# Kernel tuning notes

Hardware: AMD Instinct MI355X
Metric: run time of the kernel (lower is better)

## Reference

```python
import jax, jax.numpy as jnp
import numpy as np

N = 100_000          # nodes
E = 3_200_000        # edges (avg degree 32)
USER_SIZE = 80_000
CAT_SIZE = 5_000
USER_DIM = 8
CAT_DIM = 4
IN_CH = 8
OUT_CH = 16
HID = 16


def setup_inputs() -> dict:
    key = jax.random.key(0)
    ks = jax.random.split(key, 24)
    # features: [N,3] int; col0 = id (user id if type==0 else category id), col1 = known flag in {0,1}, col2 = type in {0,1}
    typ = jax.random.randint(ks[0], (N,), 0, 2)
    uid = jax.random.randint(ks[1], (N,), 0, USER_SIZE)
    cid = jax.random.randint(ks[2], (N,), 0, CAT_SIZE)
    col0 = jnp.where(typ == 0, uid, cid)
    col1 = jax.random.randint(ks[3], (N,), 0, 2)
    features = jnp.stack([col0, col1, typ], axis=1).astype(jnp.int64)
    edges = jax.random.randint(ks[4], (2, E), 0, N).astype(jnp.int64)

    def p(k, shape):
        return jax.random.normal(k, shape, dtype=jnp.float32) * 0.1

    return {
        "edges": edges,
        "features": features,
        "emb_user": p(ks[5], (USER_SIZE, USER_DIM)),
        "emb_known": p(ks[6], (2, USER_DIM)),
        "w_user": p(ks[7], (USER_DIM, IN_CH)),
        "b_user": p(ks[8], (IN_CH,)),
        "emb_cat": p(ks[9], (CAT_SIZE, CAT_DIM)),
        "w_cat": p(ks[10], (CAT_DIM, IN_CH)),
        "b_cat": p(ks[11], (IN_CH,)),
        "w0": p(ks[12], (IN_CH, HID)),
        "b0": p(ks[13], (HID,)),
        "w2": p(ks[14], (HID, OUT_CH)),
        "b2": p(ks[15], (OUT_CH,)),
        "w_node": p(ks[16], (OUT_CH, 2)),
        "b_node": p(ks[17], (2,)),
        "w_mem": p(ks[18], (OUT_CH, 1)),
        "b_mem": p(ks[19], (1,)),
    }


def _gcn_conv(x, w, b, src, dst, edge_norm, self_norm, n):
    h = x @ w                                      # [N, out]
    msgs = h[src] * edge_norm[:, None]             # [E, out] gather + scale
    agg = jax.ops.segment_sum(msgs, dst, num_segments=n)  # scatter-add
    agg = agg + h * self_norm[:, None]             # self-loop term
    return agg + b


def reference(edges, features, emb_user, emb_known, w_user, b_user, emb_cat,
              w_cat, b_cat, w0, b0, w2, b2, w_node, b_node, w_mem, b_mem):
    n = features.shape[0]
    typ = features[:, -1]
    is_user = (typ == 0)

    # --- input encoding (masked gather/scatter expressed as dense select) ---
    uidx = jnp.clip(features[:, 0], 0, emb_user.shape[0] - 1)
    kidx = jnp.clip(features[:, 1], 0, 1)
    cidx = jnp.clip(features[:, 0], 0, emb_cat.shape[0] - 1)
    user_f = jax.nn.relu(emb_user[uidx] + emb_known[kidx]) @ w_user + b_user
    cat_f = jax.nn.relu(emb_cat[cidx]) @ w_cat + b_cat
    x = jnp.where(is_user[:, None], user_f, cat_f)  # [N, IN_CH]

    # --- GCN normalization (shared across layers) ---
    src, dst = edges[0], edges[1]
    deg = jax.ops.segment_sum(jnp.ones((src.shape[0],), x.dtype), dst,
                              num_segments=n) + 1.0  # +1 for self-loop
    dinv = jax.lax.rsqrt(deg)
    edge_norm = dinv[src] * dinv[dst]
    self_norm = dinv * dinv

    # NOTE: original forward loop skips layers[1] entirely (enumerate over layers[:-2],
    # then applies layers[-1]); dropout branch (i>1) never triggers. Faithful here.
    h = jax.nn.relu(_gcn_conv(x, w0, b0, src, dst, edge_norm, self_norm, n))
    h = jax.nn.relu(_gcn_conv(h, w2, b2, src, dst, edge_norm, self_norm, n))

    member_pred = h @ w_mem + b_mem   # [N, 1]
    node_pred = h @ w_node + b_node   # [N, 2]
    return (member_pred, node_pred)
```

## Files before the change

### kernel.cpp

```cpp
#include <hip/hip_runtime.h>
#include <hip/hip_fp16.h>

#define BLK 256
#define PBLK 1024
#define NPB 256
#define NBSHIFT 7
#define BNODES 128
#define BMASK 127
#define NBMAX 800
#define CAP 8192
#define FXS 1048576.0f
#define FXI (1.0f / 1048576.0f)

typedef int v4i __attribute__((ext_vector_type(4)));

static inline int cdiv(int a, int b) { return (a + b - 1) / b; }

__global__ void __launch_bounds__(PBLK)
k_hist(const int* __restrict__ dst, int* __restrict__ histG, int e, int nb) {
    __shared__ int h[NBMAX];
    int tid = threadIdx.x;
    for (int t = tid; t < nb; t += PBLK) h[t] = 0;
    __syncthreads();
    int per = ((e + (int)gridDim.x - 1) / (int)gridDim.x + 3) & ~3;
    int beg = blockIdx.x * per;
    int end = min(e, beg + per);
    if (beg < end) {
        int m4 = beg + ((end - beg) & ~3);
        for (int i = beg + tid * 4; i < m4; i += PBLK * 4) {
            v4i d4 = __builtin_nontemporal_load((const v4i*)(dst + i));
            atomicAdd(&h[d4[0] >> NBSHIFT], 1);
            atomicAdd(&h[d4[1] >> NBSHIFT], 1);
            atomicAdd(&h[d4[2] >> NBSHIFT], 1);
            atomicAdd(&h[d4[3] >> NBSHIFT], 1);
        }
        int it = m4 + tid;
        if (it < end) atomicAdd(&h[dst[it] >> NBSHIFT], 1);
    }
    __syncthreads();
    for (int t = tid; t < nb; t += PBLK) histG[(size_t)blockIdx.x * nb + t] = h[t];
}

__global__ void __launch_bounds__(NPB)
k_base(const int* __restrict__ histG, int* __restrict__ baseG, int* __restrict__ tot, int nb) {
    __shared__ int s[NPB];
    int b = blockIdx.x;
    int t = threadIdx.x;
    int hc = histG[(size_t)t * nb + b];
    int r = (hc + 15) & ~15;
    s[t] = r;
    __syncthreads();
    for (int off = 1; off < NPB; off <<= 1) {
        int v = (t >= off) ? s[t - off] : 0;
        __syncthreads();
        s[t] += v;
        __syncthreads();
    }
    int excl = s[t] - r;
    baseG[(size_t)t * nb + b] = b * CAP + excl;
    if (t == NPB - 1) tot[b] = min(s[t], CAP);
}

__global__ void __launch_bounds__(PBLK)
k_scatter(const int* __restrict__ src, const int* __restrict__ dst,
          const int* __restrict__ baseG, int* __restrict__ slab, int e, int nb) {
    __shared__ int cur[NBMAX];
    int tid = threadIdx.x;
    int blk = blockIdx.x;
    for (int t = tid; t < nb; t += PBLK) cur[t] = baseG[(size_t)blk * nb + t];
    __syncthreads();
    int per = ((e + (int)gridDim.x - 1) / (int)gridDim.x + 3) & ~3;
    int beg = blk * per;
    int end = min(e, beg + per);
    if (beg < end) {
        int m4 = beg + ((end - beg) & ~3);
        for (int i = beg + tid * 4; i < m4; i += PBLK * 4) {
            v4i s4 = __builtin_nontemporal_load((const v4i*)(src + i));
            v4i d4 = __builtin_nontemporal_load((const v4i*)(dst + i));
#pragma unroll
            for (int k = 0; k < 4; ++k) {
                int d = d4[k];
                int b = d >> NBSHIFT;
                int pos = atomicAdd(&cur[b], 1);
                if (pos < (b + 1) * CAP) slab[pos] = (s4[k] << NBSHIFT) | (d & BMASK);
            }
        }
        int it = m4 + tid;
        if (it < end) {
            int d = dst[it];
            int b = d >> NBSHIFT;
            int pos = atomicAdd(&cur[b], 1);
            if (pos < (b + 1) * CAP) slab[pos] = (src[it] << NBSHIFT) | (d & BMASK);
        }
    }
    __syncthreads();
    for (int bb = tid; bb < nb; bb += PBLK) {
        int c = cur[bb];
        int lim = (bb + 1) * CAP;
        while ((c & 15) && c < lim) slab[c++] = -1;
    }
}

__global__ void __launch_bounds__(BLK)
k_bdeg(const int* __restrict__ tot, const int* __restrict__ slab,
       float* __restrict__ dinv, int n) {
    __shared__ int cnt[BNODES];
    int tid = threadIdx.x;
    if (tid < BNODES) cnt[tid] = 0;
    __syncthreads();
    int b = blockIdx.x;
    int nslots = tot[b] >> 2;
    const v4i* sl4 = reinterpret_cast<const v4i*>(slab + (size_t)b * CAP);
    for (int i = tid; i < nslots; i += BLK) {
        v4i u4 = sl4[i];
#pragma unroll
        for (int k = 0; k < 4; ++k)
            if (u4[k] >= 0) atomicAdd(&cnt[u4[k] & BMASK], 1);
    }
    __syncthreads();
    int nd = b * BNODES + tid;
    if (tid < BNODES && nd < n) dinv[nd] = rsqrtf((float)cnt[tid] + 1.0f);
}

__global__ void k_featmm(const int* __restrict__ feat,
                         const float* __restrict__ emb_user,
                         const float* __restrict__ emb_known,
                         const float* __restrict__ w_user,
                         const float* __restrict__ b_user,
                         const float* __restrict__ emb_cat,
                         const float* __restrict__ w_cat,
                         const float* __restrict__ b_cat,
                         const float* __restrict__ w0,
                         const float* __restrict__ dinv,
                         __half* __restrict__ Hs,
                         int n, int user_max, int cat_max) {
    __shared__ float w0s[8 * 16];
    for (int t = threadIdx.x; t < 8 * 16; t += blockDim.x) w0s[t] = w0[t];
    __syncthreads();
    int i = blockIdx.x * blockDim.x + threadIdx.x;
    if (i >= n) return;
    int col0 = feat[i * 3 + 0];
    int col1 = feat[i * 3 + 1];
    int typ  = feat[i * 3 + 2];
    float x[8];
    if (typ == 0) {
        int u = min(max(col0, 0), user_max);
        int k = min(max(col1, 0), 1);
        const float4* eu = reinterpret_cast<const float4*>(emb_user + (size_t)u * 8);
        const float4* ek = reinterpret_cast<const float4*>(emb_known + (size_t)k * 8);
        float4 a0 = eu[0], a1 = eu[1], k0 = ek[0], k1 = ek[1];
        float in[8];
        in[0] = fmaxf(a0.x + k0.x, 0.f); in[1] = fmaxf(a0.y + k0.y, 0.f);
        in[2] = fmaxf(a0.z + k0.z, 0.f); in[3] = fmaxf(a0.w + k0.w, 0.f);
        in[4] = fmaxf(a1.x + k1.x, 0.f); in[5] = fmaxf(a1.y + k1.y, 0.f);
        in[6] = fmaxf(a1.z + k1.z, 0.f); in[7] = fmaxf(a1.w + k1.w, 0.f);
#pragma unroll
        for (int c = 0; c < 8; ++c) {
            float s = b_user[c];
#pragma unroll
            for (int d = 0; d < 8; ++d) s += in[d] * w_user[d * 8 + c];
            x[c] = s;
        }
    } else {
        int ci = min(max(col0, 0), cat_max);
        float4 c0 = reinterpret_cast<const float4*>(emb_cat + (size_t)ci * 4)[0];
        float in[4];
        in[0] = fmaxf(c0.x, 0.f); in[1] = fmaxf(c0.y, 0.f);
        in[2] = fmaxf(c0.z, 0.f); in[3] = fmaxf(c0.w, 0.f);
#pragma unroll
        for (int c = 0; c < 8; ++c) {
            float s = b_cat[c];
#pragma unroll
            for (int d = 0; d < 4; ++d) s += in[d] * w_cat[d * 8 + c];
            x[c] = s;
        }
    }
    float dv = dinv[i];
    float o[16];
#pragma unroll
    for (int c = 0; c < 16; ++c) {
        float s = 0.f;
#pragma unroll
        for (int d = 0; d < 8; ++d) s += x[d] * w0s[d * 16 + c];
        o[c] = s * dv;
    }
    union { __half2 h[8]; uint4 u[2]; } pk;
#pragma unroll
    for (int k = 0; k < 8; ++k) pk.h[k] = __floats2half2_rn(o[2 * k], o[2 * k + 1]);
    uint4* dp = reinterpret_cast<uint4*>(Hs + (size_t)i * 16);
    dp[0] = pk.u[0];
    dp[1] = pk.u[1];
}

__device__ __forceinline__ void gather_loop(const int* __restrict__ slabb, int mtot,
                                            const uint4* __restrict__ Hs4,
                                            int (*acc)[17], int tid) {
    const v4i* sl4 = reinterpret_cast<const v4i*>(slabb);
    int nslots = mtot >> 2;
    int g = tid >> 1, q = tid & 1;
    for (int base = 0; base < nslots; base += 256) {
        int i0 = base + g;
        int i1 = base + 128 + g;
        v4i e0 = sl4[min(i0, (CAP >> 2) - 1)];
        v4i e1 = sl4[min(i1, (CAP >> 2) - 1)];
        bool b0 = i0 < nslots, b1 = i1 < nslots;
        int us[8];
        us[0] = b0 ? e0[0] : -1; us[1] = b0 ? e0[1] : -1;
        us[2] = b0 ? e0[2] : -1; us[3] = b0 ? e0[3] : -1;
        us[4] = b1 ? e1[0] : -1; us[5] = b1 ? e1[1] : -1;
        us[6] = b1 ? e1[2] : -1; us[7] = b1 ? e1[3] : -1;
        uint4 v[8];
#pragma unroll
        for (int k = 0; k < 8; ++k)
            if (us[k] >= 0) v[k] = Hs4[(size_t)(us[k] >> NBSHIFT) * 2 + q];
#pragma unroll
        for (int k = 0; k < 8; ++k) {
            if (us[k] >= 0) {
                int dl = us[k] & BMASK;
                union { uint4 u4; __half2 h[4]; } c;
                c.u4 = v[k];
#pragma unroll
                for (int j = 0; j < 4; ++j) {
                    float2 f = __half22float2(c.h[j]);
                    atomicAdd(&acc[dl][8 * q + 2 * j + 0], __float2int_rn(f.x * FXS));
                    atomicAdd(&acc[dl][8 * q + 2 * j + 1], __float2int_rn(f.y * FXS));
                }
            }
        }
    }
}

__global__ void __launch_bounds__(BLK, 4)
k_bconv1(const int* __restrict__ tot, const int* __restrict__ slab,
         const __half* __restrict__ Hs, const float* __restrict__ dinv,
         const float* __restrict__ b0, const float* __restrict__ w2,
         __half* __restrict__ Hs2, int n) {
    __shared__ int acc[BNODES][17];
    __shared__ float w2s[16 * 16];
    __shared__ float b0s[16];
    int tid = threadIdx.x;
    for (int t = tid; t < BNODES * 17; t += BLK) ((int*)acc)[t] = 0;
    w2s[tid] = w2[tid];
    if (tid < 16) b0s[tid] = b0[tid];
    __syncthreads();
    int b = blockIdx.x;
    gather_loop(slab + (size_t)b * CAP, tot[b], reinterpret_cast<const uint4*>(Hs), acc, tid);
    __syncthreads();
    int nd = b * BNODES + tid;
    if (tid < BNODES && nd < n) {
        float dv = dinv[nd];
        const __half* hrow = Hs + (size_t)nd * 16;
        float h1[16];
#pragma unroll
        for (int c = 0; c < 16; ++c) {
            float v = dv * ((float)acc[tid][c] * FXI + __half2float(hrow[c])) + b0s[c];
            h1[c] = v > 0.f ? v : 0.f;
        }
        float o[16];
#pragma unroll
        for (int c2 = 0; c2 < 16; ++c2) {
            float sum = 0.f;
#pragma unroll
            for (int c = 0; c < 16; ++c) sum += h1[c] * w2s[c * 16 + c2];
            o[c2] = sum * dv;
        }
        union { __half2 h[8]; uint4 u[2]; } pk;
#pragma unroll
        for (int k = 0; k < 8; ++k) pk.h[k] = __floats2half2_rn(o[2 * k], o[2 * k + 1]);
        uint4* dp = reinterpret_cast<uint4*>(Hs2 + (size_t)nd * 16);
        dp[0] = pk.u[0];
        dp[1] = pk.u[1];
    }
}

__global__ void __launch_bounds__(BLK, 4)
k_bconv2(const int* __restrict__ tot, const int* __restrict__ slab,
         const __half* __restrict__ Hs, const float* __restrict__ dinv,
         const float* __restrict__ b2,
         const float* __restrict__ w_mem, const float* __restrict__ b_mem,
         const float* __restrict__ w_node, const float* __restrict__ b_node,
         float* __restrict__ out, int n) {
    __shared__ int acc[BNODES][17];
    __shared__ float wms[16], wn0[16], wn1[16], b2s[16];
    int tid = threadIdx.x;
    for (int t = tid; t < BNODES * 17; t += BLK) ((int*)acc)[t] = 0;
    if (tid < 16) {
        wms[tid] = w_mem[tid];
        wn0[tid] = w_node[tid * 2 + 0];
        wn1[tid] = w_node[tid * 2 + 1];
        b2s[tid] = b2[tid];
    }
    __syncthreads();
    int b = blockIdx.x;
    gather_loop(slab + (size_t)b * CAP, tot[b], reinterpret_cast<const uint4*>(Hs), acc, tid);
    __syncthreads();
    int nd = b * BNODES + tid;
    if (tid < BNODES && nd < n) {
        float dv = dinv[nd];
        const __half* hrow = Hs + (size_t)nd * 16;
        float mph = b_mem[0];
        float n0 = b_node[0];
        float n1 = b_node[1];
#pragma unroll
        for (int c = 0; c < 16; ++c) {
            float v = dv * ((float)acc[tid][c] * FXI + __half2float(hrow[c])) + b2s[c];
            float h = v > 0.f ? v : 0.f;
            mph += h * wms[c];
            n0  += h * wn0[c];
            n1  += h * wn1[c];
        }
        out[nd] = mph;
        out[n + 2 * nd + 0] = n0;
        out[n + 2 * nd + 1] = n1;
    }
}

extern "C" void kernel_launch(void* const* d_in, const int* in_sizes, int n_in,
                              void* d_out, int out_size, void* d_ws, size_t ws_size,
                              hipStream_t stream) {
    const int*   edges     = (const int*)d_in[0];
    const int*   feat      = (const int*)d_in[1];
    const float* emb_user  = (const float*)d_in[2];
    const float* emb_known = (const float*)d_in[3];
    const float* w_user    = (const float*)d_in[4];
    const float* b_user    = (const float*)d_in[5];
    const float* emb_cat   = (const float*)d_in[6];
    const float* w_cat     = (const float*)d_in[7];
    const float* b_cat     = (const float*)d_in[8];
    const float* w0        = (const float*)d_in[9];
    const float* b0        = (const float*)d_in[10];
    const float* w2        = (const float*)d_in[11];
    const float* b2        = (const float*)d_in[12];
    const float* w_node    = (const float*)d_in[13];
    const float* b_node    = (const float*)d_in[14];
    const float* w_mem     = (const float*)d_in[15];
    const float* b_mem     = (const float*)d_in[16];

    const int E = in_sizes[0] / 2;
    const int n = in_sizes[1] / 3;
    const int user_max = in_sizes[2] / 8 - 1;
    const int cat_max  = in_sizes[6] / 4 - 1;
    const int NB = cdiv(n, BNODES);

    const int* src = edges;
    const int* dst = edges + E;

    int* slab    = (int*)d_ws;
    __half* hsA  = (__half*)(slab + (size_t)NB * CAP);
    __half* hsB  = hsA + (size_t)n * 16;
    float* dinv  = (float*)(hsB + (size_t)n * 16);
    int* histG   = (int*)(dinv + n);
    int* baseG   = histG + (size_t)NPB * NB;
    int* tot     = baseG + (size_t)NPB * NB;

    float* outp = (float*)d_out;

    k_hist<<<NPB, PBLK, 0, stream>>>(dst, histG, E, NB);
    k_base<<<NB, NPB, 0, stream>>>(histG, baseG, tot, NB);
    k_scatter<<<NPB, PBLK, 0, stream>>>(src, dst, baseG, slab, E, NB);
    k_bdeg<<<NB, BLK, 0, stream>>>(tot, slab, dinv, n);
    k_featmm<<<cdiv(n, BLK), BLK, 0, stream>>>(feat, emb_user, emb_known, w_user, b_user,
                                               emb_cat, w_cat, b_cat, w0, dinv, hsA,
                                               n, user_max, cat_max);
    k_bconv1<<<NB, BLK, 0, stream>>>(tot, slab, hsA, dinv, b0, w2, hsB, n);
    k_bconv2<<<NB, BLK, 0, stream>>>(tot, slab, hsB, dinv, b2,
                                     w_mem, b_mem, w_node, b_node, outp, n);
}
```

Measured before the change: 123.2 us.

## Bucket edges by 1024-node chunks and split consumers into 128-row slices

Edges are now sorted into coarse 1024-node destination buckets instead of 128-node buckets. This shrinks the histogram and offset arrays and cuts the per-block 16-slot padding in the scatter slab. The degree and both convolution kernels launch 8 blocks per bucket. Each block scans the whole bucket and keeps only edges whose destination falls in its 128-row slice. The cost is 8x redundant slab reads, which likely hit in cache. Launch bounds are raised to 8 waves per EU to raise occupancy.

```diff
diff --git a/kernel.cpp b/kernel.cpp
--- a/kernel.cpp
+++ b/kernel.cpp
@@ -4,11 +4,14 @@
 #define BLK 256
 #define PBLK 1024
 #define NPB 256
-#define NBSHIFT 7
-#define BNODES 128
-#define BMASK 127
-#define NBMAX 800
-#define CAP 8192
+#define CSHIFT 10
+#define CNODES 1024
+#define CMASK 1023
+#define SSHIFT 7
+#define SROWS 128
+#define SRMASK 127
+#define NBCMAX 128
+#define CAP 40960
 #define FXS 1048576.0f
 #define FXI (1.0f / 1048576.0f)
 
@@ -18,7 +21,7 @@
 
 __global__ void __launch_bounds__(PBLK)
 k_hist(const int* __restrict__ dst, int* __restrict__ histG, int e, int nb) {
-    __shared__ int h[NBMAX];
+    __shared__ int h[NBCMAX];
     int tid = threadIdx.x;
     for (int t = tid; t < nb; t += PBLK) h[t] = 0;
     __syncthreads();
@@ -29,13 +32,13 @@
         int m4 = beg + ((end - beg) & ~3);
         for (int i = beg + tid * 4; i < m4; i += PBLK * 4) {
             v4i d4 = __builtin_nontemporal_load((const v4i*)(dst + i));
-            atomicAdd(&h[d4[0] >> NBSHIFT], 1);
-            atomicAdd(&h[d4[1] >> NBSHIFT], 1);
-            atomicAdd(&h[d4[2] >> NBSHIFT], 1);
-            atomicAdd(&h[d4[3] >> NBSHIFT], 1);
+            atomicAdd(&h[d4[0] >> CSHIFT], 1);
+            atomicAdd(&h[d4[1] >> CSHIFT], 1);
+            atomicAdd(&h[d4[2] >> CSHIFT], 1);
+            atomicAdd(&h[d4[3] >> CSHIFT], 1);
         }
         int it = m4 + tid;
-        if (it < end) atomicAdd(&h[dst[it] >> NBSHIFT], 1);
+        if (it < end) atomicAdd(&h[dst[it] >> CSHIFT], 1);
     }
     __syncthreads();
     for (int t = tid; t < nb; t += PBLK) histG[(size_t)blockIdx.x * nb + t] = h[t];
@@ -64,7 +67,7 @@
 __global__ void __launch_bounds__(PBLK)
 k_scatter(const int* __restrict__ src, const int* __restrict__ dst,
           const int* __restrict__ baseG, int* __restrict__ slab, int e, int nb) {
-    __shared__ int cur[NBMAX];
+    __shared__ int cur[NBCMAX];
     int tid = threadIdx.x;
     int blk = blockIdx.x;
     for (int t = tid; t < nb; t += PBLK) cur[t] = baseG[(size_t)blk * nb + t];
@@ -80,17 +83,17 @@
 #pragma unroll
             for (int k = 0; k < 4; ++k) {
                 int d = d4[k];
-                int b = d >> NBSHIFT;
+                int b = d >> CSHIFT;
                 int pos = atomicAdd(&cur[b], 1);
-                if (pos < (b + 1) * CAP) slab[pos] = (s4[k] << NBSHIFT) | (d & BMASK);
+                if (pos < (b + 1) * CAP) slab[pos] = (s4[k] << CSHIFT) | (d & CMASK);
             }
         }
         int it = m4 + tid;
         if (it < end) {
             int d = dst[it];
-            int b = d >> NBSHIFT;
+            int b = d >> CSHIFT;
             int pos = atomicAdd(&cur[b], 1);
-            if (pos < (b + 1) * CAP) slab[pos] = (src[it] << NBSHIFT) | (d & BMASK);
+            if (pos < (b + 1) * CAP) slab[pos] = (src[it] << CSHIFT) | (d & CMASK);
         }
     }
     __syncthreads();
@@ -104,22 +107,25 @@
 __global__ void __launch_bounds__(BLK)
 k_bdeg(const int* __restrict__ tot, const int* __restrict__ slab,
        float* __restrict__ dinv, int n) {
-    __shared__ int cnt[BNODES];
-    int tid = threadIdx.x;
-    if (tid < BNODES) cnt[tid] = 0;
-    __syncthreads();
-    int b = blockIdx.x;
+    __shared__ int cnt[SROWS];
+    int tid = threadIdx.x;
+    if (tid < SROWS) cnt[tid] = 0;
+    __syncthreads();
+    int b = blockIdx.x >> 3;
+    int slice = blockIdx.x & 7;
     int nslots = tot[b] >> 2;
     const v4i* sl4 = reinterpret_cast<const v4i*>(slab + (size_t)b * CAP);
     for (int i = tid; i < nslots; i += BLK) {
         v4i u4 = sl4[i];
 #pragma unroll
-        for (int k = 0; k < 4; ++k)
-            if (u4[k] >= 0) atomicAdd(&cnt[u4[k] & BMASK], 1);
-    }
-    __syncthreads();
-    int nd = b * BNODES + tid;
-    if (tid < BNODES && nd < n) dinv[nd] = rsqrtf((float)cnt[tid] + 1.0f);
+        for (int k = 0; k < 4; ++k) {
+            int u = u4[k];
+            if (u >= 0 && ((u >> SSHIFT) & 7) == slice) atomicAdd(&cnt[u & SRMASK], 1);
+        }
+    }
+    __syncthreads();
+    int nd = b * CNODES + slice * SROWS + tid;
+    if (tid < SROWS && nd < n) dinv[nd] = rsqrtf((float)cnt[tid] + 1.0f);
 }
 
 __global__ void k_featmm(const int* __restrict__ feat,
@@ -194,7 +200,7 @@
 
 __device__ __forceinline__ void gather_loop(const int* __restrict__ slabb, int mtot,
                                             const uint4* __restrict__ Hs4,
-                                            int (*acc)[17], int tid) {
+                                            int (*acc)[17], int tid, int slice) {
     const v4i* sl4 = reinterpret_cast<const v4i*>(slabb);
     int nslots = mtot >> 2;
     int g = tid >> 1, q = tid & 1;
@@ -209,14 +215,17 @@
         us[2] = b0 ? e0[2] : -1; us[3] = b0 ? e0[3] : -1;
         us[4] = b1 ? e1[0] : -1; us[5] = b1 ? e1[1] : -1;
         us[6] = b1 ? e1[2] : -1; us[7] = b1 ? e1[3] : -1;
+#pragma unroll
+        for (int k = 0; k < 8; ++k)
+            if (us[k] >= 0 && ((us[k] >> SSHIFT) & 7) != slice) us[k] = -1;
         uint4 v[8];
 #pragma unroll
         for (int k = 0; k < 8; ++k)
-            if (us[k] >= 0) v[k] = Hs4[(size_t)(us[k] >> NBSHIFT) * 2 + q];
+            if (us[k] >= 0) v[k] = Hs4[(size_t)(us[k] >> CSHIFT) * 2 + q];
 #pragma unroll
         for (int k = 0; k < 8; ++k) {
             if (us[k] >= 0) {
-                int dl = us[k] & BMASK;
+                int dl = us[k] & SRMASK;
                 union { uint4 u4; __half2 h[4]; } c;
                 c.u4 = v[k];
 #pragma unroll
@@ -230,24 +239,26 @@
     }
 }
 
-__global__ void __launch_bounds__(BLK, 4)
+__global__ void __launch_bounds__(BLK, 8)
 k_bconv1(const int* __restrict__ tot, const int* __restrict__ slab,
          const __half* __restrict__ Hs, const float* __restrict__ dinv,
          const float* __restrict__ b0, const float* __restrict__ w2,
          __half* __restrict__ Hs2, int n) {
-    __shared__ int acc[BNODES][17];
+    __shared__ int acc[SROWS][17];
     __shared__ float w2s[16 * 16];
     __shared__ float b0s[16];
     int tid = threadIdx.x;
-    for (int t = tid; t < BNODES * 17; t += BLK) ((int*)acc)[t] = 0;
+    for (int t = tid; t < SROWS * 17; t += BLK) ((int*)acc)[t] = 0;
     w2s[tid] = w2[tid];
     if (tid < 16) b0s[tid] = b0[tid];
     __syncthreads();
-    int b = blockIdx.x;
-    gather_loop(slab + (size_t)b * CAP, tot[b], reinterpret_cast<const uint4*>(Hs), acc, tid);
-    __syncthreads();
-    int nd = b * BNODES + tid;
-    if (tid < BNODES && nd < n) {
+    int b = blockIdx.x >> 3;
+    int slice = blockIdx.x & 7;
+    gather_loop(slab + (size_t)b * CAP, tot[b], reinterpret_cast<const uint4*>(Hs),
+                acc, tid, slice);
+    __syncthreads();
+    int nd = b * CNODES + slice * SROWS + tid;
+    if (tid < SROWS && nd < n) {
         float dv = dinv[nd];
         const __half* hrow = Hs + (size_t)nd * 16;
         float h1[16];
@@ -273,17 +284,17 @@
     }
 }
 
-__global__ void __launch_bounds__(BLK, 4)
+__global__ void __launch_bounds__(BLK, 8)
 k_bconv2(const int* __restrict__ tot, const int* __restrict__ slab,
          const __half* __restrict__ Hs, const float* __restrict__ dinv,
          const float* __restrict__ b2,
          const float* __restrict__ w_mem, const float* __restrict__ b_mem,
          const float* __restrict__ w_node, const float* __restrict__ b_node,
          float* __restrict__ out, int n) {
-    __shared__ int acc[BNODES][17];
+    __shared__ int acc[SROWS][17];
     __shared__ float wms[16], wn0[16], wn1[16], b2s[16];
     int tid = threadIdx.x;
-    for (int t = tid; t < BNODES * 17; t += BLK) ((int*)acc)[t] = 0;
+    for (int t = tid; t < SROWS * 17; t += BLK) ((int*)acc)[t] = 0;
     if (tid < 16) {
         wms[tid] = w_mem[tid];
         wn0[tid] = w_node[tid * 2 + 0];
@@ -291,11 +302,13 @@
         b2s[tid] = b2[tid];
     }
     __syncthreads();
-    int b = blockIdx.x;
-    gather_loop(slab + (size_t)b * CAP, tot[b], reinterpret_cast<const uint4*>(Hs), acc, tid);
-    __syncthreads();
-    int nd = b * BNODES + tid;
-    if (tid < BNODES && nd < n) {
+    int b = blockIdx.x >> 3;
+    int slice = blockIdx.x & 7;
+    gather_loop(slab + (size_t)b * CAP, tot[b], reinterpret_cast<const uint4*>(Hs),
+                acc, tid, slice);
+    __syncthreads();
+    int nd = b * CNODES + slice * SROWS + tid;
+    if (tid < SROWS && nd < n) {
         float dv = dinv[nd];
         const __half* hrow = Hs + (size_t)nd * 16;
         float mph = b_mem[0];
@@ -340,29 +353,29 @@
     const int n = in_sizes[1] / 3;
     const int user_max = in_sizes[2] / 8 - 1;
     const int cat_max  = in_sizes[6] / 4 - 1;
-    const int NB = cdiv(n, BNODES);
+    const int NBC = cdiv(n, CNODES);
 
     const int* src = edges;
     const int* dst = edges + E;
 
     int* slab    = (int*)d_ws;
-    __half* hsA  = (__half*)(slab + (size_t)NB * CAP);
+    __half* hsA  = (__half*)(slab + (size_t)NBC * CAP);
     __half* hsB  = hsA + (size_t)n * 16;
     float* dinv  = (float*)(hsB + (size_t)n * 16);
     int* histG   = (int*)(dinv + n);
-    int* baseG   = histG + (size_t)NPB * NB;
-    int* tot     = baseG + (size_t)NPB * NB;
+    int* baseG   = histG + (size_t)NPB * NBC;
+    int* tot     = baseG + (size_t)NPB * NBC;
 
     float* outp = (float*)d_out;
 
-    k_hist<<<NPB, PBLK, 0, stream>>>(dst, histG, E, NB);
-    k_base<<<NB, NPB, 0, stream>>>(histG, baseG, tot, NB);
-    k_scatter<<<NPB, PBLK, 0, stream>>>(src, dst, baseG, slab, E, NB);
-    k_bdeg<<<NB, BLK, 0, stream>>>(tot, slab, dinv, n);
+    k_hist<<<NPB, PBLK, 0, stream>>>(dst, histG, E, NBC);
+    k_base<<<NBC, NPB, 0, stream>>>(histG, baseG, tot, NBC);
+    k_scatter<<<NPB, PBLK, 0, stream>>>(src, dst, baseG, slab, E, NBC);
+    k_bdeg<<<NBC * 8, BLK, 0, stream>>>(tot, slab, dinv, n);
     k_featmm<<<cdiv(n, BLK), BLK, 0, stream>>>(feat, emb_user, emb_known, w_user, b_user,
                                                emb_cat, w_cat, b_cat, w0, dinv, hsA,
                                                n, user_max, cat_max);
-    k_bconv1<<<NB, BLK, 0, stream>>>(tot, slab, hsA, dinv, b0, w2, hsB, n);
-    k_bconv2<<<NB, BLK, 0, stream>>>(tot, slab, hsB, dinv, b2,
-                                     w_mem, b_mem, w_node, b_node, outp, n);
-}
+    k_bconv1<<<NBC * 8, BLK, 0, stream>>>(tot, slab, hsA, dinv, b0, w2, hsB, n);
+    k_bconv2<<<NBC * 8, BLK, 0, stream>>>(tot, slab, hsB, dinv, b2,
+                                          w_mem, b_mem, w_node, b_node, outp, n);
+}
```

Measured after the change: 265.0 us. +115.1%, slower.
